# Performance work log

Measured on AMD Instinct MI355X. Metric: run time of the kernel, lower is better.

The kernel has to match this reference:

```python
import jax, jax.numpy as jnp
import numpy as np

SUPPORT = 8
NEIGH = 32
EPS = 1e-6


def setup_inputs() -> dict:
    key = jax.random.key(0)
    xyz = jax.random.normal(key, (4, 4096, 3), dtype=jnp.float32)
    return {"xyz": xyz}


def _gather(points, idx):
    # points: (B, N, D), idx: (B, N, K) -> (B, N, K, D)
    return jax.vmap(lambda p, i: p[i])(points, idx)


def _forward(xyz):
    B, N, _ = xyz.shape
    # brute-force squared pairwise distances (B, N, N)
    sq = jnp.sum(xyz * xyz, axis=-1)
    d = sq[:, :, None] + sq[:, None, :] - 2.0 * jnp.einsum('bnd,bmd->bnm', xyz, xyz)
    # k nearest neighbors, ascending distance; idx[...,0] is the point itself
    _, idx = jax.lax.top_k(-d, NEIGH)  # (B, N, NEIGH)

    # --- PCA normal estimation (pytorch3d estimate_pointcloud_normals) ---
    nbrs = _gather(xyz, idx)                      # (B, N, K, 3)
    ctr = nbrs.mean(axis=2, keepdims=True)
    X = nbrs - ctr
    cov = jnp.einsum('bnki,bnkj->bnij', X, X)     # (B, N, 3, 3)
    _, v = jnp.linalg.eigh(cov)                   # eigenvalues ascending
    normals = v[..., :, 0]                        # eigenvector of smallest eigenvalue
    # disambiguate direction: flip so normal agrees with offsets to neighbors
    df = nbrs - xyz[:, :, None, :]                # (B, N, K, 3)
    proj = jnp.einsum('bnd,bnkd->bnk', normals, df).sum(-1)
    normals = jnp.where((proj < 0.0)[..., None], -normals, normals)  # (B, N, 3)

    # --- KNN (support) gather of normals; same metric, sorted, so slice ---
    idx_s = idx[..., :SUPPORT]                    # (B, N, S)
    nn_normals = _gather(normals, idx_s)          # (B, N, S, 3)

    # cosine similarity between self normal and each neighbor normal
    anchor = nn_normals[:, :, 0:1, :]             # (B, N, 1, 3)
    na = jnp.maximum(jnp.linalg.norm(anchor, axis=-1), EPS)
    nb = jnp.maximum(jnp.linalg.norm(nn_normals, axis=-1), EPS)
    cos = jnp.sum(anchor * nn_normals, axis=-1) / (na * nb)  # (B, N, S)

    penalty = 1.0 - cos
    penalty = penalty.std(axis=-1, ddof=1)        # torch .std default unbiased
    return penalty.mean(axis=-1)                  # (B,)


def reference(xyz):
    return _forward(xyz)
```

## Files before the change

kernel.cpp:

```cpp
#include <hip/hip_runtime.h>

typedef unsigned int uint;

#define NPTS 4096
#define BLK  256
#define KNN  32
#define KSUP 8
#define NBIN 1024
#define MAXC 256
#define LINSCALE 16.0f

__global__ __launch_bounds__(256) void pack_kernel(
        const float* __restrict__ xyz, float4* __restrict__ pts4, int total)
{
    int i = blockIdx.x * BLK + threadIdx.x;
    if (i < total) {
        float x = xyz[i*3+0], y = xyz[i*3+1], z = xyz[i*3+2];
        pts4[i] = make_float4(x, y, z, x*x + y*y + z*z);
    }
}

__device__ __forceinline__ uint fkey(float d) {
    uint u = __float_as_uint(d);
    return u ^ ((u & 0x80000000u) ? 0xFFFFFFFFu : 0x80000000u);
}
__device__ __forceinline__ float key_to_d(uint k) {
    uint u = (k & 0x80000000u) ? (k ^ 0x80000000u) : ~k;
    return __uint_as_float(u);
}
__device__ __forceinline__ uint linbin(float d) {
    return (uint)fmaxf(fminf(d * LINSCALE, 1023.0f), 0.0f);
}

__device__ __forceinline__ void find_cross(const uint* hist, uint* s_bin, int tid) {
    if (tid < 64) {
        const uint4* h4 = (const uint4*)hist;
        uint4 h0 = h4[tid*4+0], h1 = h4[tid*4+1], h2 = h4[tid*4+2], h3 = h4[tid*4+3];
        uint s = h0.x+h0.y+h0.z+h0.w + h1.x+h1.y+h1.z+h1.w
               + h2.x+h2.y+h2.z+h2.w + h3.x+h3.y+h3.z+h3.w;
        uint t = s;
        #pragma unroll
        for (int off = 1; off < 64; off <<= 1) {
            uint u = __shfl_up(t, off, 64);
            if (tid >= off) t += u;
        }
        uint ex = t - s;
        if (ex < KNN && ex + s >= KNN) {
            uint cum = ex, binoff = 0;
            cum += h0.x; binoff += (cum < KNN); cum += h0.y; binoff += (cum < KNN);
            cum += h0.z; binoff += (cum < KNN); cum += h0.w; binoff += (cum < KNN);
            cum += h1.x; binoff += (cum < KNN); cum += h1.y; binoff += (cum < KNN);
            cum += h1.z; binoff += (cum < KNN); cum += h1.w; binoff += (cum < KNN);
            cum += h2.x; binoff += (cum < KNN); cum += h2.y; binoff += (cum < KNN);
            cum += h2.z; binoff += (cum < KNN); cum += h2.w; binoff += (cum < KNN);
            cum += h3.x; binoff += (cum < KNN); cum += h3.y; binoff += (cum < KNN);
            cum += h3.z; binoff += (cum < KNN); cum += h3.w; binoff += (cum < KNN);
            *s_bin = tid * 16u + binoff;
        }
    }
}

__global__ __launch_bounds__(256) void knn_cov_kernel(
        const float4* __restrict__ pts4,
        float* __restrict__ covS,
        int*   __restrict__ idx8)
{
    const int pid = blockIdx.x;
    const int b   = pid >> 12;
    const int n   = pid & (NPTS - 1);
    const int tid = threadIdx.x;
    const float4* P = pts4 + (size_t)b * NPTS;

    __shared__ uint keys[NPTS];
    __shared__ uint hist[NBIN];
    __shared__ uint s_bin;
    __shared__ uint s_mode;
    __shared__ uint coll_cnt;
    __shared__ uint ckey[MAXC];
    __shared__ int  cidx[MAXC];
    __shared__ int  sel[KNN];

    const float4 q = P[n];
    const float qx = q.x, qy = q.y, qz = q.z, sqn = q.w;

    #pragma unroll
    for (int i = 0; i < NBIN / BLK; ++i) hist[tid + i * BLK] = 0;
    if (tid == 0) { coll_cnt = 0; s_mode = 0; }
    __syncthreads();

    #pragma unroll 4
    for (int m = tid; m < NPTS; m += BLK) {
        float4 p = P[m];
        float d = sqn + p.w - 2.0f * (qx * p.x + qy * p.y + qz * p.z);
        keys[m] = fkey(d);
        atomicAdd(&hist[linbin(d)], 1u);
    }
    __syncthreads();

    find_cross(hist, &s_bin, tid);
    __syncthreads();
    if (tid == 0 && s_bin == 1023u) s_mode = 1u;
    __syncthreads();

    if (s_mode) {
        #pragma unroll
        for (int i = 0; i < NBIN / BLK; ++i) hist[tid + i * BLK] = 0;
        __syncthreads();
        for (int m = tid; m < NPTS; m += BLK) atomicAdd(&hist[keys[m] >> 22], 1u);
        __syncthreads();
        find_cross(hist, &s_bin, tid);
        __syncthreads();
    }
    const uint bmax = s_bin;
    const uint mode = s_mode;

    for (int m = tid; m < NPTS; m += BLK) {
        uint k = keys[m];
        uint bin = mode ? (k >> 22) : linbin(key_to_d(k));
        if (bin <= bmax) {
            uint pos = atomicAdd(&coll_cnt, 1u);
            if (pos < MAXC) { ckey[pos] = k; cidx[pos] = m; }
        }
    }
    __syncthreads();
    const int M = (int)min(coll_cnt, (uint)MAXC);

    for (int i = tid; i < M; i += BLK) {
        uint uk = ckey[i]; int ui = cidx[i];
        int r = 0;
        for (int j = 0; j < M; ++j) {
            uint vk = ckey[j];
            r += (vk < uk || (vk == uk && cidx[j] < ui)) ? 1 : 0;
        }
        if (r < KNN) sel[r] = ui;
    }
    __syncthreads();

    if (tid < 32) {
        int j = sel[tid];
        float4 pj = P[j];
        float q0 = pj.x, q1 = pj.y, q2 = pj.z;

        float s0 = q0, s1 = q1, s2 = q2;
        #pragma unroll
        for (int ml = 1; ml < 32; ml <<= 1) {
            s0 += __shfl_xor(s0, ml, 32);
            s1 += __shfl_xor(s1, ml, 32);
            s2 += __shfl_xor(s2, ml, 32);
        }
        const float c0 = s0 * (1.0f/32.0f), c1 = s1 * (1.0f/32.0f), c2 = s2 * (1.0f/32.0f);
        const float X0 = q0 - c0, X1 = q1 - c1, X2 = q2 - c2;
        float xx = X0*X0, xy = X0*X1, xz = X0*X2, yy = X1*X1, yz = X1*X2, zz = X2*X2;
        #pragma unroll
        for (int ml = 1; ml < 32; ml <<= 1) {
            xx += __shfl_xor(xx, ml, 32);
            xy += __shfl_xor(xy, ml, 32);
            xz += __shfl_xor(xz, ml, 32);
            yy += __shfl_xor(yy, ml, 32);
            yz += __shfl_xor(yz, ml, 32);
            zz += __shfl_xor(zz, ml, 32);
        }
        if (tid == 0) {
            float4* o = (float4*)(covS + (size_t)pid * 12);
            o[0] = make_float4(xx, xy, xz, yy);
            o[1] = make_float4(yz, zz, s0 - 32.0f*qx, s1 - 32.0f*qy);
            o[2] = make_float4(s2 - 32.0f*qz, 0.0f, 0.0f, 0.0f);
        }
    }
    if (tid < KSUP) idx8[(size_t)pid*KSUP + tid] = sel[tid];
}

__global__ __launch_bounds__(256) void eig_kernel(
        const float* __restrict__ covS, float* __restrict__ normals, int total)
{
    const int pid = blockIdx.x * BLK + threadIdx.x;
    if (pid >= total) return;
    const float4* c4 = (const float4*)(covS + (size_t)pid * 12);
    const float4 a = c4[0], bb = c4[1], cc = c4[2];

    double A00 = a.x, A01 = a.y, A02 = a.z, A11 = a.w, A12 = bb.x, A22 = bb.y;
    const float S0 = bb.z, S1 = bb.w, S2 = cc.x;
    double V00=1, V01=0, V02=0, V10=0, V11=1, V12=0, V20=0, V21=0, V22=1;

    #pragma unroll
    for (int sweep = 0; sweep < 5; ++sweep) {
        {
            double apq = A01;
            if (fabs(apq) > 1e-300) {
                double th = (A11 - A00) / (2.0*apq);
                double t  = (th >= 0.0 ? 1.0 : -1.0) / (fabs(th) + sqrt(th*th + 1.0));
                double c  = 1.0/sqrt(t*t + 1.0), s = t*c;
                double a00 = c*c*A00 - 2.0*s*c*A01 + s*s*A11;
                double a11 = s*s*A00 + 2.0*s*c*A01 + c*c*A11;
                double a02 = c*A02 - s*A12;
                double a12 = s*A02 + c*A12;
                A00 = a00; A11 = a11; A01 = 0.0; A02 = a02; A12 = a12;
                double v0, v1;
                v0 = V00; v1 = V01; V00 = c*v0 - s*v1; V01 = s*v0 + c*v1;
                v0 = V10; v1 = V11; V10 = c*v0 - s*v1; V11 = s*v0 + c*v1;
                v0 = V20; v1 = V21; V20 = c*v0 - s*v1; V21 = s*v0 + c*v1;
            }
        }
        {
            double apq = A02;
            if (fabs(apq) > 1e-300) {
                double th = (A22 - A00) / (2.0*apq);
                double t  = (th >= 0.0 ? 1.0 : -1.0) / (fabs(th) + sqrt(th*th + 1.0));
                double c  = 1.0/sqrt(t*t + 1.0), s = t*c;
                double a00 = c*c*A00 - 2.0*s*c*A02 + s*s*A22;
                double a22 = s*s*A00 + 2.0*s*c*A02 + c*c*A22;
                double a01 = c*A01 - s*A12;
                double a12 = s*A01 + c*A12;
                A00 = a00; A22 = a22; A02 = 0.0; A01 = a01; A12 = a12;
                double v0, v1;
                v0 = V00; v1 = V02; V00 = c*v0 - s*v1; V02 = s*v0 + c*v1;
                v0 = V10; v1 = V12; V10 = c*v0 - s*v1; V12 = s*v0 + c*v1;
                v0 = V20; v1 = V22; V20 = c*v0 - s*v1; V22 = s*v0 + c*v1;
            }
        }
        {
            double apq = A12;
            if (fabs(apq) > 1e-300) {
                double th = (A22 - A11) / (2.0*apq);
                double t  = (th >= 0.0 ? 1.0 : -1.0) / (fabs(th) + sqrt(th*th + 1.0));
                double c  = 1.0/sqrt(t*t + 1.0), s = t*c;
                double a11 = c*c*A11 - 2.0*s*c*A12 + s*s*A22;
                double a22 = s*s*A11 + 2.0*s*c*A12 + c*c*A22;
                double a01 = c*A01 - s*A02;
                double a02 = s*A01 + c*A02;
                A11 = a11; A22 = a22; A12 = 0.0; A01 = a01; A02 = a02;
                double v0, v1;
                v0 = V01; v1 = V02; V01 = c*v0 - s*v1; V02 = s*v0 + c*v1;
                v0 = V11; v1 = V12; V11 = c*v0 - s*v1; V12 = s*v0 + c*v1;
                v0 = V21; v1 = V22; V21 = c*v0 - s*v1; V22 = s*v0 + c*v1;
            }
        }
    }

    double e0 = A00, e1 = A11, e2 = A22;
    double v0, v1, v2;
    if (e0 <= e1 && e0 <= e2)      { v0 = V00; v1 = V10; v2 = V20; }
    else if (e1 <= e0 && e1 <= e2) { v0 = V01; v1 = V11; v2 = V21; }
    else                           { v0 = V02; v1 = V12; v2 = V22; }
    double nrm = sqrt(v0*v0 + v1*v1 + v2*v2);
    if (nrm > 0.0) { v0 /= nrm; v1 /= nrm; v2 /= nrm; }

    float f0 = (float)v0, f1 = (float)v1, f2 = (float)v2;
    float proj = f0*S0 + f1*S1 + f2*S2;
    if (proj < 0.0f) { f0 = -f0; f1 = -f1; f2 = -f2; }
    normals[(size_t)pid*3+0] = f0;
    normals[(size_t)pid*3+1] = f1;
    normals[(size_t)pid*3+2] = f2;
}

__global__ __launch_bounds__(256) void penalty_kernel(
        const float* __restrict__ normals,
        const int*   __restrict__ idx8,
        float*       __restrict__ out)
{
    const int pid = blockIdx.x * BLK + threadIdx.x;
    const int b   = pid >> 12;
    const int* my = idx8 + (size_t)pid * KSUP;
    const float* nb_base = normals + (size_t)b * NPTS * 3;

    const int i0 = my[0];
    const float a0 = nb_base[i0*3+0], a1 = nb_base[i0*3+1], a2 = nb_base[i0*3+2];
    const float na = fmaxf(sqrtf(a0*a0 + a1*a1 + a2*a2), 1e-6f);

    float p[KSUP];
    float sum = 0.0f;
    #pragma unroll
    for (int k = 0; k < KSUP; ++k) {
        int ik = my[k];
        float b0 = nb_base[ik*3+0], b1 = nb_base[ik*3+1], b2 = nb_base[ik*3+2];
        float nbn = fmaxf(sqrtf(b0*b0 + b1*b1 + b2*b2), 1e-6f);
        float cosv = (a0*b0 + a1*b1 + a2*b2) / (na * nbn);
        p[k] = 1.0f - cosv;
        sum += p[k];
    }
    const float mean = sum * (1.0f / 8.0f);
    float var = 0.0f;
    #pragma unroll
    for (int k = 0; k < KSUP; ++k) { float dv = p[k] - mean; var += dv * dv; }
    float v = sqrtf(var * (1.0f / 7.0f)) * (1.0f / 4096.0f);

    #pragma unroll
    for (int ml = 1; ml < 64; ml <<= 1) v += __shfl_xor(v, ml, 64);
    __shared__ float red[4];
    if ((threadIdx.x & 63) == 0) red[threadIdx.x >> 6] = v;
    __syncthreads();
    if (threadIdx.x == 0) {
        atomicAdd(&out[b], red[0] + red[1] + red[2] + red[3]);
    }
}

extern "C" void kernel_launch(void* const* d_in, const int* in_sizes, int n_in,
                              void* d_out, int out_size, void* d_ws, size_t ws_size,
                              hipStream_t stream) {
    const float* xyz = (const float*)d_in[0];
    float* out = (float*)d_out;

    const int B = in_sizes[0] / (NPTS * 3);
    const int total = B * NPTS;

    char* ws = (char*)d_ws;
    float4* pts4   = (float4*)ws;                       ws += (size_t)total * sizeof(float4);
    float*  covS   = (float*)ws;                        ws += (size_t)total * 12 * sizeof(float);
    float*  normals= (float*)ws;                        ws += (size_t)total * 3 * sizeof(float);
    int*    idx8   = (int*)ws;

    hipMemsetAsync(d_out, 0, (size_t)out_size * sizeof(float), stream);

    hipLaunchKernelGGL(pack_kernel, dim3((total + BLK - 1) / BLK), dim3(BLK), 0, stream,
                       xyz, pts4, total);
    hipLaunchKernelGGL(knn_cov_kernel, dim3(total), dim3(BLK), 0, stream,
                       pts4, covS, idx8);
    hipLaunchKernelGGL(eig_kernel, dim3((total + BLK - 1) / BLK), dim3(BLK), 0, stream,
                       covS, normals, total);
    hipLaunchKernelGGL(penalty_kernel, dim3(total / BLK), dim3(BLK), 0, stream,
                       normals, idx8, out);
}
```

Before: 150.3 us.

## Predict KNN distance threshold analytically, fall back to histogram selection

Each query point now gets a candidate distance threshold estimated from its squared norm, and candidates are collected in a single pass without building a histogram. The 16KB shared keys array is removed, which cuts LDS use and may raise occupancy. If the candidate count falls outside [KNN, MAXC], the kernel recomputes distances and runs the original linear or radix histogram selection. MAXC is raised to 352 to hold more candidates, at the cost of a larger O(M^2) rank step. The threshold formula is tuned to Gaussian-like point clouds, but the fallback keeps results exact for other inputs.

```diff
diff --git a/kernel.cpp b/kernel.cpp
--- a/kernel.cpp
+++ b/kernel.cpp
@@ -7,7 +7,7 @@
 #define KNN  32
 #define KSUP 8
 #define NBIN 1024
-#define MAXC 256
+#define MAXC 352
 #define LINSCALE 16.0f
 
 __global__ __launch_bounds__(256) void pack_kernel(
@@ -23,10 +23,6 @@
 __device__ __forceinline__ uint fkey(float d) {
     uint u = __float_as_uint(d);
     return u ^ ((u & 0x80000000u) ? 0xFFFFFFFFu : 0x80000000u);
-}
-__device__ __forceinline__ float key_to_d(uint k) {
-    uint u = (k & 0x80000000u) ? (k ^ 0x80000000u) : ~k;
-    return __uint_as_float(u);
 }
 __device__ __forceinline__ uint linbin(float d) {
     return (uint)fmaxf(fminf(d * LINSCALE, 1023.0f), 0.0f);
@@ -71,7 +67,6 @@
     const int tid = threadIdx.x;
     const float4* P = pts4 + (size_t)b * NPTS;
 
-    __shared__ uint keys[NPTS];
     __shared__ uint hist[NBIN];
     __shared__ uint s_bin;
     __shared__ uint s_mode;
@@ -83,8 +78,8 @@
     const float4 q = P[n];
     const float qx = q.x, qy = q.y, qz = q.z, sqn = q.w;
 
-    #pragma unroll
-    for (int i = 0; i < NBIN / BLK; ++i) hist[tid + i * BLK] = 0;
+    const float t0 = 0.1606f * __expf(sqn * (1.0f / 3.0f));
+
     if (tid == 0) { coll_cnt = 0; s_mode = 0; }
     __syncthreads();
 
@@ -92,37 +87,56 @@
     for (int m = tid; m < NPTS; m += BLK) {
         float4 p = P[m];
         float d = sqn + p.w - 2.0f * (qx * p.x + qy * p.y + qz * p.z);
-        keys[m] = fkey(d);
-        atomicAdd(&hist[linbin(d)], 1u);
+        if (d < t0) {
+            uint pos = atomicAdd(&coll_cnt, 1u);
+            if (pos < MAXC) { ckey[pos] = fkey(d); cidx[pos] = m; }
+        }
     }
     __syncthreads();
 
-    find_cross(hist, &s_bin, tid);
-    __syncthreads();
-    if (tid == 0 && s_bin == 1023u) s_mode = 1u;
-    __syncthreads();
-
-    if (s_mode) {
+    uint cnt = coll_cnt;
+    if (cnt < KNN || cnt > MAXC) {
+        if (tid == 0) { s_mode = 1; coll_cnt = 0; }
         #pragma unroll
         for (int i = 0; i < NBIN / BLK; ++i) hist[tid + i * BLK] = 0;
         __syncthreads();
-        for (int m = tid; m < NPTS; m += BLK) atomicAdd(&hist[keys[m] >> 22], 1u);
+
+        #pragma unroll 4
+        for (int m = tid; m < NPTS; m += BLK) {
+            float4 p = P[m];
+            float d = sqn + p.w - 2.0f * (qx * p.x + qy * p.y + qz * p.z);
+            atomicAdd(&hist[linbin(d)], 1u);
+        }
         __syncthreads();
         find_cross(hist, &s_bin, tid);
         __syncthreads();
-    }
-    const uint bmax = s_bin;
-    const uint mode = s_mode;
-
-    for (int m = tid; m < NPTS; m += BLK) {
-        uint k = keys[m];
-        uint bin = mode ? (k >> 22) : linbin(key_to_d(k));
-        if (bin <= bmax) {
-            uint pos = atomicAdd(&coll_cnt, 1u);
-            if (pos < MAXC) { ckey[pos] = k; cidx[pos] = m; }
-        }
-    }
-    __syncthreads();
+        uint lin_ok = (s_bin != 1023u);
+        if (!lin_ok) {
+            #pragma unroll
+            for (int i = 0; i < NBIN / BLK; ++i) hist[tid + i * BLK] = 0;
+            __syncthreads();
+            for (int m = tid; m < NPTS; m += BLK) {
+                float4 p = P[m];
+                float d = sqn + p.w - 2.0f * (qx * p.x + qy * p.y + qz * p.z);
+                atomicAdd(&hist[fkey(d) >> 22], 1u);
+            }
+            __syncthreads();
+            find_cross(hist, &s_bin, tid);
+            __syncthreads();
+        }
+        const uint bmax = s_bin;
+        for (int m = tid; m < NPTS; m += BLK) {
+            float4 p = P[m];
+            float d = sqn + p.w - 2.0f * (qx * p.x + qy * p.y + qz * p.z);
+            uint k = fkey(d);
+            uint bin = lin_ok ? linbin(d) : (k >> 22);
+            if (bin <= bmax) {
+                uint pos = atomicAdd(&coll_cnt, 1u);
+                if (pos < MAXC) { ckey[pos] = k; cidx[pos] = m; }
+            }
+        }
+        __syncthreads();
+    }
     const int M = (int)min(coll_cnt, (uint)MAXC);
 
     for (int i = tid; i < M; i += BLK) {
```

After: 154.6 us. 1.03x slower.

## Replace histogram KNN selection with per-wave threshold ballot compaction

Applied to the files above, without the earlier changes.

Each 64-lane wave now handles one query point, four queries per block, instead of one 256-thread block per query. Selection uses a distance threshold estimated from the point's norm, retried up to eight times, with ballot/mbcnt compaction into a small LDS buffer, then a rank sort of packed key|index values. If no threshold works, it falls back to 32 rounds of iterative minimum. This drops the 16KB key array, the histogram atomics and the block-wide barriers, but the threshold formula is tuned to Gaussian inputs and a retry means another full pass over the points. The memset is folded into pack_kernel, and the small kernels move to 64-thread blocks.

```diff
diff --git a/kernel.cpp b/kernel.cpp
--- a/kernel.cpp
+++ b/kernel.cpp
@@ -1,63 +1,29 @@
 #include <hip/hip_runtime.h>
 
 typedef unsigned int uint;
+typedef unsigned long long u64;
 
 #define NPTS 4096
-#define BLK  256
 #define KNN  32
 #define KSUP 8
-#define NBIN 1024
-#define MAXC 256
-#define LINSCALE 16.0f
-
-__global__ __launch_bounds__(256) void pack_kernel(
-        const float* __restrict__ xyz, float4* __restrict__ pts4, int total)
-{
-    int i = blockIdx.x * BLK + threadIdx.x;
+#define QPB  4
+#define MAXCQ 192
+
+__global__ __launch_bounds__(64) void pack_kernel(
+        const float* __restrict__ xyz, float4* __restrict__ pts4, int total,
+        float* __restrict__ out, int nout)
+{
+    int i = blockIdx.x * 64 + threadIdx.x;
     if (i < total) {
         float x = xyz[i*3+0], y = xyz[i*3+1], z = xyz[i*3+2];
         pts4[i] = make_float4(x, y, z, x*x + y*y + z*z);
     }
+    if (blockIdx.x == 0 && threadIdx.x < nout) out[threadIdx.x] = 0.0f;
 }
 
 __device__ __forceinline__ uint fkey(float d) {
     uint u = __float_as_uint(d);
     return u ^ ((u & 0x80000000u) ? 0xFFFFFFFFu : 0x80000000u);
-}
-__device__ __forceinline__ float key_to_d(uint k) {
-    uint u = (k & 0x80000000u) ? (k ^ 0x80000000u) : ~k;
-    return __uint_as_float(u);
-}
-__device__ __forceinline__ uint linbin(float d) {
-    return (uint)fmaxf(fminf(d * LINSCALE, 1023.0f), 0.0f);
-}
-
-__device__ __forceinline__ void find_cross(const uint* hist, uint* s_bin, int tid) {
-    if (tid < 64) {
-        const uint4* h4 = (const uint4*)hist;
-        uint4 h0 = h4[tid*4+0], h1 = h4[tid*4+1], h2 = h4[tid*4+2], h3 = h4[tid*4+3];
-        uint s = h0.x+h0.y+h0.z+h0.w + h1.x+h1.y+h1.z+h1.w
-               + h2.x+h2.y+h2.z+h2.w + h3.x+h3.y+h3.z+h3.w;
-        uint t = s;
-        #pragma unroll
-        for (int off = 1; off < 64; off <<= 1) {
-            uint u = __shfl_up(t, off, 64);
-            if (tid >= off) t += u;
-        }
-        uint ex = t - s;
-        if (ex < KNN && ex + s >= KNN) {
-            uint cum = ex, binoff = 0;
-            cum += h0.x; binoff += (cum < KNN); cum += h0.y; binoff += (cum < KNN);
-            cum += h0.z; binoff += (cum < KNN); cum += h0.w; binoff += (cum < KNN);
-            cum += h1.x; binoff += (cum < KNN); cum += h1.y; binoff += (cum < KNN);
-            cum += h1.z; binoff += (cum < KNN); cum += h1.w; binoff += (cum < KNN);
-            cum += h2.x; binoff += (cum < KNN); cum += h2.y; binoff += (cum < KNN);
-            cum += h2.z; binoff += (cum < KNN); cum += h2.w; binoff += (cum < KNN);
-            cum += h3.x; binoff += (cum < KNN); cum += h3.y; binoff += (cum < KNN);
-            cum += h3.z; binoff += (cum < KNN); cum += h3.w; binoff += (cum < KNN);
-            *s_bin = tid * 16u + binoff;
-        }
-    }
 }
 
 __global__ __launch_bounds__(256) void knn_cov_kernel(
@@ -65,83 +31,82 @@
         float* __restrict__ covS,
         int*   __restrict__ idx8)
 {
-    const int pid = blockIdx.x;
-    const int b   = pid >> 12;
-    const int n   = pid & (NPTS - 1);
-    const int tid = threadIdx.x;
+    const int tid  = threadIdx.x;
+    const int g    = tid >> 6;
+    const int lane = tid & 63;
+    const int bid  = blockIdx.x;
+    const int b    = bid / (NPTS / QPB);
+    const int n    = (bid % (NPTS / QPB)) * QPB + g;
+    const int pid  = b * NPTS + n;
     const float4* P = pts4 + (size_t)b * NPTS;
 
-    __shared__ uint keys[NPTS];
-    __shared__ uint hist[NBIN];
-    __shared__ uint s_bin;
-    __shared__ uint s_mode;
-    __shared__ uint coll_cnt;
-    __shared__ uint ckey[MAXC];
-    __shared__ int  cidx[MAXC];
-    __shared__ int  sel[KNN];
+    __shared__ u64 cand[QPB][MAXCQ];
+    __shared__ int sel[QPB][KNN];
 
     const float4 q = P[n];
     const float qx = q.x, qy = q.y, qz = q.z, sqn = q.w;
-
-    #pragma unroll
-    for (int i = 0; i < NBIN / BLK; ++i) hist[tid + i * BLK] = 0;
-    if (tid == 0) { coll_cnt = 0; s_mode = 0; }
+    float t = 0.1606f * __expf(sqn * (1.0f / 3.0f));
+
+    uint cnt = 0;
+    bool ok = false;
+    for (int attempt = 0; attempt < 8 && !ok; ++attempt) {
+        cnt = 0;
+        #pragma unroll 4
+        for (int k0 = 0; k0 < NPTS; k0 += 64) {
+            const int k = k0 + lane;
+            float4 p = P[k];
+            float d = sqn + p.w - 2.0f * (qx * p.x + qy * p.y + qz * p.z);
+            bool pred = d < t;
+            u64 mask = __ballot(pred);
+            if (pred) {
+                uint pos = cnt + __builtin_amdgcn_mbcnt_hi((uint)(mask >> 32),
+                            __builtin_amdgcn_mbcnt_lo((uint)mask, 0u));
+                if (pos < MAXCQ) cand[g][pos] = ((u64)fkey(d) << 12) | (uint)k;
+            }
+            cnt += (uint)__popcll(mask);
+        }
+        if (cnt >= KNN && cnt <= MAXCQ) ok = true;
+        else t = (cnt < KNN) ? t * 2.2f : t * 0.5f;
+    }
+
+    if (ok) {
+        const int M = (int)cnt;
+        const int rounds = (M + 63) >> 6;
+        for (int rr = 0; rr < rounds; ++rr) {
+            const int i = rr * 64 + lane;
+            u64 my = (i < M) ? cand[g][i] : ~0ull;
+            int r = 0;
+            for (int j = 0; j < M; ++j) r += (cand[g][j] < my) ? 1 : 0;
+            if (i < M && r < KNN) sel[g][r] = (int)(my & 0xFFFull);
+        }
+    } else {
+        u64 last = 0;
+        for (int r = 0; r < KNN; ++r) {
+            u64 best = ~0ull;
+            for (int k0 = 0; k0 < NPTS; k0 += 64) {
+                const int k = k0 + lane;
+                float4 p = P[k];
+                float d = sqn + p.w - 2.0f * (qx * p.x + qy * p.y + qz * p.z);
+                u64 pk = ((u64)fkey(d) << 12) | (uint)k;
+                if (pk > last && pk < best) best = pk;
+            }
+            #pragma unroll
+            for (int off = 32; off; off >>= 1) {
+                u64 o = __shfl_xor(best, off, 64);
+                best = (o < best) ? o : best;
+            }
+            if (lane == 0) sel[g][r] = (int)(best & 0xFFFull);
+            last = best;
+        }
+    }
     __syncthreads();
 
-    #pragma unroll 4
-    for (int m = tid; m < NPTS; m += BLK) {
-        float4 p = P[m];
-        float d = sqn + p.w - 2.0f * (qx * p.x + qy * p.y + qz * p.z);
-        keys[m] = fkey(d);
-        atomicAdd(&hist[linbin(d)], 1u);
-    }
-    __syncthreads();
-
-    find_cross(hist, &s_bin, tid);
-    __syncthreads();
-    if (tid == 0 && s_bin == 1023u) s_mode = 1u;
-    __syncthreads();
-
-    if (s_mode) {
-        #pragma unroll
-        for (int i = 0; i < NBIN / BLK; ++i) hist[tid + i * BLK] = 0;
-        __syncthreads();
-        for (int m = tid; m < NPTS; m += BLK) atomicAdd(&hist[keys[m] >> 22], 1u);
-        __syncthreads();
-        find_cross(hist, &s_bin, tid);
-        __syncthreads();
-    }
-    const uint bmax = s_bin;
-    const uint mode = s_mode;
-
-    for (int m = tid; m < NPTS; m += BLK) {
-        uint k = keys[m];
-        uint bin = mode ? (k >> 22) : linbin(key_to_d(k));
-        if (bin <= bmax) {
-            uint pos = atomicAdd(&coll_cnt, 1u);
-            if (pos < MAXC) { ckey[pos] = k; cidx[pos] = m; }
-        }
-    }
-    __syncthreads();
-    const int M = (int)min(coll_cnt, (uint)MAXC);
-
-    for (int i = tid; i < M; i += BLK) {
-        uint uk = ckey[i]; int ui = cidx[i];
-        int r = 0;
-        for (int j = 0; j < M; ++j) {
-            uint vk = ckey[j];
-            r += (vk < uk || (vk == uk && cidx[j] < ui)) ? 1 : 0;
-        }
-        if (r < KNN) sel[r] = ui;
-    }
-    __syncthreads();
-
-    if (tid < 32) {
-        int j = sel[tid];
-        float4 pj = P[j];
-        float q0 = pj.x, q1 = pj.y, q2 = pj.z;
-
-        float s0 = q0, s1 = q1, s2 = q2;
+    if (lane < 32) {
+        const int jn = sel[g][lane];
+        float4 pj = P[jn];
+        float p0 = pj.x, p1 = pj.y, p2 = pj.z;
+
+        float s0 = p0, s1 = p1, s2 = p2;
         #pragma unroll
         for (int ml = 1; ml < 32; ml <<= 1) {
             s0 += __shfl_xor(s0, ml, 32);
@@ -149,7 +114,7 @@
             s2 += __shfl_xor(s2, ml, 32);
         }
         const float c0 = s0 * (1.0f/32.0f), c1 = s1 * (1.0f/32.0f), c2 = s2 * (1.0f/32.0f);
-        const float X0 = q0 - c0, X1 = q1 - c1, X2 = q2 - c2;
+        const float X0 = p0 - c0, X1 = p1 - c1, X2 = p2 - c2;
         float xx = X0*X0, xy = X0*X1, xz = X0*X2, yy = X1*X1, yz = X1*X2, zz = X2*X2;
         #pragma unroll
         for (int ml = 1; ml < 32; ml <<= 1) {
@@ -160,20 +125,20 @@
             yz += __shfl_xor(yz, ml, 32);
             zz += __shfl_xor(zz, ml, 32);
         }
-        if (tid == 0) {
+        if (lane == 0) {
             float4* o = (float4*)(covS + (size_t)pid * 12);
             o[0] = make_float4(xx, xy, xz, yy);
             o[1] = make_float4(yz, zz, s0 - 32.0f*qx, s1 - 32.0f*qy);
             o[2] = make_float4(s2 - 32.0f*qz, 0.0f, 0.0f, 0.0f);
         }
     }
-    if (tid < KSUP) idx8[(size_t)pid*KSUP + tid] = sel[tid];
-}
-
-__global__ __launch_bounds__(256) void eig_kernel(
+    if (lane < KSUP) idx8[(size_t)pid*KSUP + lane] = sel[g][lane];
+}
+
+__global__ __launch_bounds__(64) void eig_kernel(
         const float* __restrict__ covS, float* __restrict__ normals, int total)
 {
-    const int pid = blockIdx.x * BLK + threadIdx.x;
+    const int pid = blockIdx.x * 64 + threadIdx.x;
     if (pid >= total) return;
     const float4* c4 = (const float4*)(covS + (size_t)pid * 12);
     const float4 a = c4[0], bb = c4[1], cc = c4[2];
@@ -253,12 +218,12 @@
     normals[(size_t)pid*3+2] = f2;
 }
 
-__global__ __launch_bounds__(256) void penalty_kernel(
+__global__ __launch_bounds__(64) void penalty_kernel(
         const float* __restrict__ normals,
         const int*   __restrict__ idx8,
         float*       __restrict__ out)
 {
-    const int pid = blockIdx.x * BLK + threadIdx.x;
+    const int pid = blockIdx.x * 64 + threadIdx.x;
     const int b   = pid >> 12;
     const int* my = idx8 + (size_t)pid * KSUP;
     const float* nb_base = normals + (size_t)b * NPTS * 3;
@@ -286,12 +251,7 @@
 
     #pragma unroll
     for (int ml = 1; ml < 64; ml <<= 1) v += __shfl_xor(v, ml, 64);
-    __shared__ float red[4];
-    if ((threadIdx.x & 63) == 0) red[threadIdx.x >> 6] = v;
-    __syncthreads();
-    if (threadIdx.x == 0) {
-        atomicAdd(&out[b], red[0] + red[1] + red[2] + red[3]);
-    }
+    if (threadIdx.x == 0) atomicAdd(&out[b], v);
 }
 
 extern "C" void kernel_launch(void* const* d_in, const int* in_sizes, int n_in,
@@ -309,14 +269,12 @@
     float*  normals= (float*)ws;                        ws += (size_t)total * 3 * sizeof(float);
     int*    idx8   = (int*)ws;
 
-    hipMemsetAsync(d_out, 0, (size_t)out_size * sizeof(float), stream);
-
-    hipLaunchKernelGGL(pack_kernel, dim3((total + BLK - 1) / BLK), dim3(BLK), 0, stream,
-                       xyz, pts4, total);
-    hipLaunchKernelGGL(knn_cov_kernel, dim3(total), dim3(BLK), 0, stream,
+    hipLaunchKernelGGL(pack_kernel, dim3((total + 63) / 64), dim3(64), 0, stream,
+                       xyz, pts4, total, out, out_size);
+    hipLaunchKernelGGL(knn_cov_kernel, dim3(total / QPB), dim3(256), 0, stream,
                        pts4, covS, idx8);
-    hipLaunchKernelGGL(eig_kernel, dim3((total + BLK - 1) / BLK), dim3(BLK), 0, stream,
+    hipLaunchKernelGGL(eig_kernel, dim3((total + 63) / 64), dim3(64), 0, stream,
                        covS, normals, total);
-    hipLaunchKernelGGL(penalty_kernel, dim3(total / BLK), dim3(BLK), 0, stream,
+    hipLaunchKernelGGL(penalty_kernel, dim3(total / 64), dim3(64), 0, stream,
                        normals, idx8, out);
 }
```

Result: slower. 175.4 us (+16.7%).
